# Kernel tuning notes

Measured on AMD Instinct MI355X. Metric: run time of the kernel, lower is better.

## Reference

```python
import jax, jax.numpy as jnp
import numpy as np
import math

SR = 96000.0
FRAME = 2048
NB = 16
GAIN_RANGE = (-24.0, 24.0)
Q_RANGE = (0.5, 16.0)
BROADBAND = (-60.0, 0.0)
HPF_R = (20.0, 500.0)
LPF_R = (5000.0, 20000.0)
SHELF_R = (50.0, 16000.0)
PEAK_R = (100.0, 15000.0)


def _dfreq(n, rng):
    lo, hi = math.log(rng[0]), math.log(rng[1])
    return jnp.exp(lo + n * (hi - lo))


def _dgain(n, rng=GAIN_RANGE):
    return rng[0] + n * (rng[1] - rng[0])


def _dq(n):
    lo, hi = math.log(Q_RANGE[0]), math.log(Q_RANGE[1])
    return jnp.exp(lo + n * (hi - lo))


def _coeffs(ftype, fc, gain_db, Q):
    # returns stacked [g, k, a1, a2, a3, m0, m1, m2], each same shape as fc
    g = jnp.clip(jnp.tan(math.pi * fc / SR), 1e-6, 100.0)
    Q = jnp.clip(Q, 0.1, 100.0)
    one = jnp.ones_like(g)
    zero = jnp.zeros_like(g)
    if ftype in ('highpass', 'lowpass'):
        k = 1.0 / Q
        a1 = 1.0 / (1.0 + g * (g + k)); a2 = g * a1; a3 = g * a2
        if ftype == 'highpass':
            m0, m1, m2 = one, -k, -one
        else:
            m0, m1, m2 = zero, zero, one
    elif ftype == 'peak':
        A = jnp.power(10.0, gain_db / 40.0)
        k = jnp.where(gain_db >= 0, 1.0 / (Q * A), A / Q)
        a1 = 1.0 / (1.0 + g * (g + k)); a2 = g * a1; a3 = g * a2
        m0, m1, m2 = one, k * (A * A - 1.0), zero
    elif ftype == 'lowshelf':
        A = jnp.power(10.0, gain_db / 40.0); sA = jnp.sqrt(A); k = 1.0 / Q
        gs = jnp.where(gain_db >= 0, g / sA, g * sA)
        a1 = 1.0 / (1.0 + gs * (gs + k)); a2 = gs * a1; a3 = gs * a2
        m0, m1, m2 = one, k * (A - 1.0), A * A - 1.0
    else:  # highshelf
        A = jnp.power(10.0, gain_db / 40.0); sA = jnp.sqrt(A); k = 1.0 / Q
        gs = jnp.where(gain_db >= 0, g * sA, g / sA)
        a1 = 1.0 / (1.0 + gs * (gs + k)); a2 = gs * a1; a3 = gs * a2
        m0, m1, m2 = A * A, k * (1.0 - A) * A, 1.0 - A * A
    return jnp.stack([g, k, a1, a2, a3, m0, m1, m2], 0)


def _all_coeffs(params, n_frames_audio):
    # params: (B, 50, n_frames_params) -> coeffs (nF, NB, 8, B), in/out gains (nF, B)
    B = params.shape[0]
    nFp = params.shape[2]
    pidx = jnp.minimum(jnp.arange(n_frames_audio), nFp - 1)
    fp = jnp.take(params, pidx, axis=2)                 # (B, 50, nF)
    bq = fp[:, :NB * 3, :].reshape(B, NB, 3, n_frames_audio)
    in_g = jnp.power(10.0, _dgain(fp[:, -2, :], BROADBAND) / 20.0)   # (B, nF)
    out_g = jnp.power(10.0, _dgain(fp[:, -1, :], BROADBAND) / 20.0)  # (B, nF)
    cs = []
    for i in range(NB):
        fn, gn, qn = bq[:, i, 0], bq[:, i, 1], bq[:, i, 2]  # (B, nF)
        Q = _dq(qn)
        if i == 0:
            c = _coeffs('highpass', _dfreq(fn, HPF_R), None, Q)
        elif i == 15:
            c = _coeffs('lowpass', _dfreq(fn, LPF_R), None, Q)
        elif i == 1:
            c = _coeffs('lowshelf', _dfreq(fn, SHELF_R), _dgain(gn), Q)
        elif i == 14:
            c = _coeffs('highshelf', _dfreq(fn, SHELF_R), _dgain(gn), Q)
        else:
            c = _coeffs('peak', _dfreq(fn, PEAK_R), _dgain(gn), Q)
        cs.append(c)  # (8, B, nF)
    coeffs = jnp.transpose(jnp.stack(cs, 0), (3, 0, 1, 2))  # (nF, NB, 8, B)
    return coeffs, in_g.T, out_g.T


def _forward(audio, params):
    B, S = audio.shape
    nF = S // FRAME  # S chosen as exact multiple of FRAME
    coeffs, in_g, out_g = _all_coeffs(params, nF)
    frames = jnp.transpose(audio.reshape(B, nF, FRAME), (1, 2, 0))  # (nF, FRAME, B)

    def frame_step(states, xs):
        fr, c, ig, og = xs  # fr (FRAME,B), c (NB,8,B), ig (B,), og (B,)
        x = fr * ig[None, :]
        new_states = []
        for i in range(NB):
            a1, a2, a3 = c[i, 2], c[i, 3], c[i, 4]
            m0, m1, m2 = c[i, 5], c[i, 6], c[i, 7]

            def samp(st, xn, a1=a1, a2=a2, a3=a3, m0=m0, m1=m1, m2=m2):
                ic1, ic2 = st
                v3 = xn - ic2
                v1 = a1 * ic1 + a2 * v3
                v2 = ic2 + a2 * v1 + a3 * v3
                out = m0 * xn + m1 * v1 + m2 * v2
                return (2.0 * v1 - ic1, 2.0 * v2 - ic2), out

            (ic1, ic2), x = jax.lax.scan(samp, (states[i, 0], states[i, 1]), x)
            new_states.append(jnp.stack([ic1, ic2], 0))
        return jnp.stack(new_states, 0), x * og[None, :]

    init = jnp.zeros((NB, 2, B), audio.dtype)
    _, out = jax.lax.scan(frame_step, init, (frames, coeffs, in_g, out_g))
    return jnp.transpose(out, (2, 0, 1)).reshape(B, S)  # (B, S)


_forward_jit = jax.jit(_forward)


def setup_inputs() -> dict:
    key = jax.random.key(0)
    k1, k2 = jax.random.split(key)
    B, S, nFp = 32, 49152, 24  # 24 frames of 2048 samples
    audio = jax.random.normal(k1, (B, S), dtype=jnp.float32) * 0.1
    params = jax.random.uniform(k2, (B, 50, nFp), dtype=jnp.float32)
    return {'audio': audio, 'params': params}


def reference(audio, params):
    return _forward_jit(audio, params)
```

## Files before the change

kernel.cpp:

```cpp
#include <hip/hip_runtime.h>
#include <math.h>

#define NBATCH 32
#define S      49152
#define NF     24
#define NB     16
#define NBLK   4
#define CHUNK  16
#define NCH    768
#define NWAVE  12

__device__ __forceinline__ float clampf(float x, float lo, float hi) {
    return fminf(fmaxf(x, lo), hi);
}

#define FOREACH_S(OP) \
    OP(s00) OP(s01) OP(s02) OP(s03) OP(s04) OP(s05) OP(s06) OP(s07) \
    OP(s08) OP(s09) OP(s10) OP(s11) OP(s12) OP(s13) OP(s14) OP(s15)

#define DECL_S(x) float x;

#define STEPA(x) { \
    const float n1_ = fmaf(t00, ic1, fmaf(t01, ic2, b0 * (x))); \
    const float n2_ = fmaf(t10, ic1, fmaf(t11, ic2, b1 * (x))); \
    ic1 = n1_; ic2 = n2_; }

#define STEPC(x) { \
    const float y_  = fmaf(c0, ic1, fmaf(c1, ic2, c2 * (x))); \
    const float n1_ = fmaf(t00, ic1, fmaf(t01, ic2, b0 * (x))); \
    const float n2_ = fmaf(t10, ic1, fmaf(t11, ic2, b1 * (x))); \
    (x) = y_; ic1 = n1_; ic2 = n2_; }

__global__ __launch_bounds__(NCH, 3)
void biquad_chain_kernel(const float* __restrict__ audio,
                         const float* __restrict__ params,
                         float* __restrict__ out,
                         unsigned int* __restrict__ ws)
{
    __shared__ float sc[NB][NF][16];
    __shared__ float sgain[2][NF];
    __shared__ float4 saggM[NWAVE];
    __shared__ float  saggC[NWAVE][2];
    __shared__ float  sv[NWAVE][2];

    const int t       = threadIdx.x;
    const int xcd     = blockIdx.x & 7;
    const int slot_   = blockIdx.x >> 3;
    const int bt      = xcd * 4 + (slot_ & 3);
    const int quarter = slot_ >> 2;
    const int lane    = t & 63;
    const int wave    = t >> 6;
    const int frame   = quarter * 6 + (wave >> 1);

    if (t < NB * NF) {
        const int f  = t / NF;
        const int fr = t % NF;
        const float* P = params + (size_t)bt * 50 * NF;
        const float fn = P[(3 * f + 0) * NF + fr];
        const float gn = P[(3 * f + 1) * NF + fr];
        const float qn = P[(3 * f + 2) * NF + fr];

        float Q = __expf(-0.69314718f + qn * 3.4657359f);
        Q = clampf(Q, 0.1f, 100.0f);

        float lo, hi;
        int type;
        if      (f == 0)  { lo = 20.0f;   hi = 500.0f;   type = 0; }
        else if (f == 15) { lo = 5000.0f; hi = 20000.0f; type = 1; }
        else if (f == 1)  { lo = 50.0f;   hi = 16000.0f; type = 3; }
        else if (f == 14) { lo = 50.0f;   hi = 16000.0f; type = 4; }
        else              { lo = 100.0f;  hi = 15000.0f; type = 2; }

        const float fc = __expf(__logf(lo) + fn * (__logf(hi) - __logf(lo)));
        float g_ = __tanf((float)M_PI * fc / 96000.0f);
        g_ = clampf(g_, 1e-6f, 100.0f);
        const float gdb = -24.0f + 48.0f * gn;

        float a1, a2, a3, m0, m1, m2;
        if (type == 0 || type == 1) {
            const float k = 1.0f / Q;
            a1 = 1.0f / (1.0f + g_ * (g_ + k)); a2 = g_ * a1; a3 = g_ * a2;
            if (type == 0) { m0 = 1.0f; m1 = -k;   m2 = -1.0f; }
            else           { m0 = 0.0f; m1 = 0.0f; m2 = 1.0f;  }
        } else if (type == 2) {
            const float A = __expf(gdb * (2.30258509f / 40.0f));
            const float k = (gdb >= 0.0f) ? 1.0f / (Q * A) : A / Q;
            a1 = 1.0f / (1.0f + g_ * (g_ + k)); a2 = g_ * a1; a3 = g_ * a2;
            m0 = 1.0f; m1 = k * (A * A - 1.0f); m2 = 0.0f;
        } else {
            const float A  = __expf(gdb * (2.30258509f / 40.0f));
            const float sA = sqrtf(A);
            const float k  = 1.0f / Q;
            float gs;
            if (type == 3) gs = (gdb >= 0.0f) ? g_ / sA : g_ * sA;
            else           gs = (gdb >= 0.0f) ? g_ * sA : g_ / sA;
            a1 = 1.0f / (1.0f + gs * (gs + k)); a2 = gs * a1; a3 = gs * a2;
            if (type == 3) { m0 = 1.0f;  m1 = k * (A - 1.0f);      m2 = A * A - 1.0f; }
            else           { m0 = A * A; m1 = k * (1.0f - A) * A;  m2 = 1.0f - A * A; }
        }

        const float q2  = a2 * a2 + a3;
        const float t00 = 2.0f * a1 - 1.0f;
        const float t01 = -2.0f * a2;
        const float t10 = 2.0f * a1 * a2;
        const float t11 = 1.0f - 2.0f * q2;
        const float b0  = 2.0f * a2;
        const float b1  = 2.0f * q2;
        const float c0  = a1 * (m1 + m2 * a2);
        const float c1  = m2 * (1.0f - q2) - m1 * a2;
        const float c2  = m0 + m1 * a2 + m2 * q2;

        float u00 = t00, u01 = t01, u10 = t10, u11 = t11;
        #pragma unroll
        for (int i = 0; i < 4; i++) {
            const float n00 = u00 * u00 + u01 * u10;
            const float n01 = u00 * u01 + u01 * u11;
            const float n10 = u10 * u00 + u11 * u10;
            const float n11 = u10 * u01 + u11 * u11;
            u00 = n00; u01 = n01; u10 = n10; u11 = n11;
        }

        sc[f][fr][0] = t00; sc[f][fr][1] = t01; sc[f][fr][2] = t10; sc[f][fr][3] = t11;
        sc[f][fr][4] = b0;  sc[f][fr][5] = b1;  sc[f][fr][6] = c0;  sc[f][fr][7] = c1;
        sc[f][fr][8] = c2;  sc[f][fr][9] = u00; sc[f][fr][10] = u01; sc[f][fr][11] = u10;
        sc[f][fr][12] = u11;
    }
    if (t >= 384 && t < 384 + 2 * NF) {
        const int idx = t - 384;
        const int which = idx / NF;
        const int fr    = idx % NF;
        const float* P = params + (size_t)bt * 50 * NF;
        const float p  = P[(48 + which) * NF + fr];
        const float db = -60.0f + 60.0f * p;
        sgain[which][fr] = __expf(db * (2.30258509f / 20.0f));
    }
    __syncthreads();

    FOREACH_S(DECL_S)
    {
        const float ing = sgain[0][frame];
        const float* base = audio + (size_t)bt * S
                          + (size_t)(quarter * NCH + t) * CHUNK;
        float4 q;
        q = *(const float4*)(base +  0); s00 = q.x*ing; s01 = q.y*ing; s02 = q.z*ing; s03 = q.w*ing;
        q = *(const float4*)(base +  4); s04 = q.x*ing; s05 = q.y*ing; s06 = q.z*ing; s07 = q.w*ing;
        q = *(const float4*)(base +  8); s08 = q.x*ing; s09 = q.y*ing; s10 = q.z*ing; s11 = q.w*ing;
        q = *(const float4*)(base + 12); s12 = q.x*ing; s13 = q.y*ing; s14 = q.z*ing; s15 = q.w*ing;
    }

    #pragma unroll 1
    for (int f = 0; f < NB; f++) {
        const float4 q0 = *(const float4*)&sc[f][frame][0];
        const float4 q1 = *(const float4*)&sc[f][frame][4];
        const float4 q2 = *(const float4*)&sc[f][frame][8];
        const float  M11v = sc[f][frame][12];
        const float t00 = q0.x, t01 = q0.y, t10 = q0.z, t11 = q0.w;
        const float b0  = q1.x, b1  = q1.y, c0  = q1.z, c1  = q1.w;
        const float c2  = q2.x;

        float ic1 = 0.0f, ic2 = 0.0f;
        FOREACH_S(STEPA)

        float Md00 = q2.y, Md01 = q2.z, Md10 = q2.w, Md11 = M11v;
        float Ac0 = ic1, Ac1 = ic2;
        #pragma unroll
        for (int d = 1; d < 64; d <<= 1) {
            const float lc0 = __shfl_up(Ac0, d);
            const float lc1 = __shfl_up(Ac1, d);
            if (lane >= d) {
                Ac0 = fmaf(Md00, lc0, fmaf(Md01, lc1, Ac0));
                Ac1 = fmaf(Md10, lc0, fmaf(Md11, lc1, Ac1));
            }
            const float n00 = Md00 * Md00 + Md01 * Md10;
            const float n01 = Md00 * Md01 + Md01 * Md11;
            const float n10 = Md10 * Md00 + Md11 * Md10;
            const float n11 = Md10 * Md01 + Md11 * Md11;
            Md00 = n00; Md01 = n01; Md10 = n10; Md11 = n11;
        }

        if (lane == 63) {
            saggM[wave] = make_float4(Md00, Md01, Md10, Md11);
            saggC[wave][0] = Ac0; saggC[wave][1] = Ac1;
        }
        __syncthreads();

        const unsigned int tag = (unsigned int)(f + 1);
        unsigned int* stagebase = ws + ((bt * NB + f) * NBLK) * 8;

        if (wave == 0) {
            float G00 = 1.0f, G01 = 0.0f, G10 = 0.0f, G11 = 1.0f, Gc0 = 0.0f, Gc1 = 0.0f;
            if (lane < NWAVE) {
                const float4 m = saggM[lane];
                G00 = m.x; G01 = m.y; G10 = m.z; G11 = m.w;
                Gc0 = saggC[lane][0]; Gc1 = saggC[lane][1];
            }
            #pragma unroll
            for (int d = 1; d < 16; d <<= 1) {
                const float l00 = __shfl_up(G00, d);
                const float l01 = __shfl_up(G01, d);
                const float l10 = __shfl_up(G10, d);
                const float l11 = __shfl_up(G11, d);
                const float lc0 = __shfl_up(Gc0, d);
                const float lc1 = __shfl_up(Gc1, d);
                if (lane >= d && lane < NWAVE) {
                    const float n00 = G00 * l00 + G01 * l10;
                    const float n01 = G00 * l01 + G01 * l11;
                    const float n10 = G10 * l00 + G11 * l10;
                    const float n11 = G10 * l01 + G11 * l11;
                    const float nc0 = G00 * lc0 + G01 * lc1 + Gc0;
                    const float nc1 = G10 * lc0 + G11 * lc1 + Gc1;
                    G00 = n00; G01 = n01; G10 = n10; G11 = n11;
                    Gc0 = nc0; Gc1 = nc1;
                }
            }

            if (quarter < NBLK - 1 && lane == NWAVE - 1) {
                unsigned int* slot = stagebase + quarter * 8;
                float* dp = (float*)(slot + 1);
                __hip_atomic_store(&dp[0], G00, __ATOMIC_RELAXED, __HIP_MEMORY_SCOPE_AGENT);
                __hip_atomic_store(&dp[1], G01, __ATOMIC_RELAXED, __HIP_MEMORY_SCOPE_AGENT);
                __hip_atomic_store(&dp[2], G10, __ATOMIC_RELAXED, __HIP_MEMORY_SCOPE_AGENT);
                __hip_atomic_store(&dp[3], G11, __ATOMIC_RELAXED, __HIP_MEMORY_SCOPE_AGENT);
                __hip_atomic_store(&dp[4], Gc0, __ATOMIC_RELAXED, __HIP_MEMORY_SCOPE_AGENT);
                __hip_atomic_store(&dp[5], Gc1, __ATOMIC_RELAXED, __HIP_MEMORY_SCOPE_AGENT);
                __hip_atomic_store(slot, tag, __ATOMIC_RELEASE, __HIP_MEMORY_SCOPE_AGENT);
            }

            float P00 = __shfl_up(G00, 1);
            float P01 = __shfl_up(G01, 1);
            float P10 = __shfl_up(G10, 1);
            float P11 = __shfl_up(G11, 1);
            float Pc0 = __shfl_up(Gc0, 1);
            float Pc1 = __shfl_up(Gc1, 1);
            if (lane == 0) { P00 = 1.0f; P01 = 0.0f; P10 = 0.0f; P11 = 1.0f; Pc0 = 0.0f; Pc1 = 0.0f; }

            float S0x = 0.0f, S0y = 0.0f;
            if (lane == 0 && quarter > 0) {
                float sx = 0.0f, sy = 0.0f;
                for (int k2 = 0; k2 < quarter; k2++) {
                    unsigned int* slot = stagebase + k2 * 8;
                    while (__hip_atomic_load(slot, __ATOMIC_ACQUIRE, __HIP_MEMORY_SCOPE_AGENT) != tag) {
                        __builtin_amdgcn_s_sleep(1);
                    }
                    float* dp = (float*)(slot + 1);
                    const float m00 = __hip_atomic_load(&dp[0], __ATOMIC_RELAXED, __HIP_MEMORY_SCOPE_AGENT);
                    const float m01 = __hip_atomic_load(&dp[1], __ATOMIC_RELAXED, __HIP_MEMORY_SCOPE_AGENT);
                    const float m10 = __hip_atomic_load(&dp[2], __ATOMIC_RELAXED, __HIP_MEMORY_SCOPE_AGENT);
                    const float m11 = __hip_atomic_load(&dp[3], __ATOMIC_RELAXED, __HIP_MEMORY_SCOPE_AGENT);
                    const float cc0 = __hip_atomic_load(&dp[4], __ATOMIC_RELAXED, __HIP_MEMORY_SCOPE_AGENT);
                    const float cc1 = __hip_atomic_load(&dp[5], __ATOMIC_RELAXED, __HIP_MEMORY_SCOPE_AGENT);
                    const float nx = m00 * sx + m01 * sy + cc0;
                    const float ny = m10 * sx + m11 * sy + cc1;
                    sx = nx; sy = ny;
                }
                S0x = sx; S0y = sy;
            }
            S0x = __shfl(S0x, 0);
            S0y = __shfl(S0y, 0);

            if (lane < NWAVE) {
                sv[lane][0] = fmaf(P00, S0x, fmaf(P01, S0y, Pc0));
                sv[lane][1] = fmaf(P10, S0x, fmaf(P11, S0y, Pc1));
            }
        }
        __syncthreads();

        const float vx = sv[wave][0];
        const float vy = sv[wave][1];

        float ce0 = __shfl_up(Ac0, 1);
        float ce1 = __shfl_up(Ac1, 1);
        if (lane == 0) { ce0 = 0.0f; ce1 = 0.0f; }

        float w0 = vx, w1 = vy;
        float p00 = q2.y, p01 = q2.z, p10 = q2.w, p11 = M11v;
        #pragma unroll
        for (int b = 0; b < 6; b++) {
            if (lane & (1 << b)) {
                const float nw0 = fmaf(p00, w0, p01 * w1);
                const float nw1 = fmaf(p10, w0, p11 * w1);
                w0 = nw0; w1 = nw1;
            }
            if (b < 5) {
                const float n00 = p00 * p00 + p01 * p10;
                const float n01 = p00 * p01 + p01 * p11;
                const float n10 = p10 * p00 + p11 * p10;
                const float n11 = p10 * p01 + p11 * p11;
                p00 = n00; p01 = n01; p10 = n10; p11 = n11;
            }
        }
        ic1 = w0 + ce0;
        ic2 = w1 + ce1;

        FOREACH_S(STEPC)
    }

    {
        const float og = sgain[1][frame];
        float* base = out + (size_t)bt * S + (size_t)(quarter * NCH + t) * CHUNK;
        float4 q;
        q.x = s00*og; q.y = s01*og; q.z = s02*og; q.w = s03*og; *(float4*)(base +  0) = q;
        q.x = s04*og; q.y = s05*og; q.z = s06*og; q.w = s07*og; *(float4*)(base +  4) = q;
        q.x = s08*og; q.y = s09*og; q.z = s10*og; q.w = s11*og; *(float4*)(base +  8) = q;
        q.x = s12*og; q.y = s13*og; q.z = s14*og; q.w = s15*og; *(float4*)(base + 12) = q;
    }
}

extern "C" void kernel_launch(void* const* d_in, const int* in_sizes, int n_in,
                              void* d_out, int out_size, void* d_ws, size_t ws_size,
                              hipStream_t stream)
{
    const float* audio  = (const float*)d_in[0];
    const float* params = (const float*)d_in[1];
    float* out = (float*)d_out;
    unsigned int* ws = (unsigned int*)d_ws;
    biquad_chain_kernel<<<NBLK * NBATCH, NCH, 0, stream>>>(audio, params, out, ws);
}
```

Before: 124.8 us.

## Fuse biquad sections pairwise into 4-state block-triangular scan

New measurement: 128.5 us. +3.0%, slower.

```diff
diff --git a/kernel.cpp b/kernel.cpp
--- a/kernel.cpp
+++ b/kernel.cpp
@@ -5,6 +5,7 @@
 #define S      49152
 #define NF     24
 #define NB     16
+#define NPAIR  8
 #define NBLK   4
 #define CHUNK  16
 #define NCH    768
@@ -20,16 +21,44 @@
 
 #define DECL_S(x) float x;
 
-#define STEPA(x) { \
-    const float n1_ = fmaf(t00, ic1, fmaf(t01, ic2, b0 * (x))); \
-    const float n2_ = fmaf(t10, ic1, fmaf(t11, ic2, b1 * (x))); \
-    ic1 = n1_; ic2 = n2_; }
-
-#define STEPC(x) { \
-    const float y_  = fmaf(c0, ic1, fmaf(c1, ic2, c2 * (x))); \
-    const float n1_ = fmaf(t00, ic1, fmaf(t01, ic2, b0 * (x))); \
-    const float n2_ = fmaf(t10, ic1, fmaf(t11, ic2, b1 * (x))); \
-    (x) = y_; ic1 = n1_; ic2 = n2_; }
+#define STEPA2(x) { \
+    const float y1_ = fmaf(c0f, zu, fmaf(c1f, zw, c2f * (x))); \
+    const float nu_ = fmaf(tf00, zu, fmaf(tf01, zw, bf0 * (x))); \
+    const float nw_ = fmaf(tf10, zu, fmaf(tf11, zw, bf1 * (x))); \
+    const float ng_ = fmaf(tg00, zg, fmaf(tg01, zh, bg0 * y1_)); \
+    const float nh_ = fmaf(tg10, zg, fmaf(tg11, zh, bg1 * y1_)); \
+    zu = nu_; zw = nw_; zg = ng_; zh = nh_; }
+
+#define STEPC2(x) { \
+    const float y1_ = fmaf(c0f, zu, fmaf(c1f, zw, c2f * (x))); \
+    const float y2_ = fmaf(c0g, zg, fmaf(c1g, zh, c2g * y1_)); \
+    const float nu_ = fmaf(tf00, zu, fmaf(tf01, zw, bf0 * (x))); \
+    const float nw_ = fmaf(tf10, zu, fmaf(tf11, zw, bf1 * (x))); \
+    const float ng_ = fmaf(tg00, zg, fmaf(tg01, zh, bg0 * y1_)); \
+    const float nh_ = fmaf(tg10, zg, fmaf(tg11, zh, bg1 * y1_)); \
+    (x) = y2_; zu = nu_; zw = nw_; zg = ng_; zh = nh_; }
+
+__device__ __forceinline__ void tri_sq(
+    float& a00, float& a01, float& a10, float& a11,
+    float& b00, float& b01, float& b10, float& b11,
+    float& d00, float& d01, float& d10, float& d11)
+{
+    const float na00 = a00*a00 + a01*a10;
+    const float na01 = a00*a01 + a01*a11;
+    const float na10 = a10*a00 + a11*a10;
+    const float na11 = a10*a01 + a11*a11;
+    const float nb00 = b00*a00 + b01*a10 + d00*b00 + d01*b10;
+    const float nb01 = b00*a01 + b01*a11 + d00*b01 + d01*b11;
+    const float nb10 = b10*a00 + b11*a10 + d10*b00 + d11*b10;
+    const float nb11 = b10*a01 + b11*a11 + d10*b01 + d11*b11;
+    const float nd00 = d00*d00 + d01*d10;
+    const float nd01 = d00*d01 + d01*d11;
+    const float nd10 = d10*d00 + d11*d10;
+    const float nd11 = d10*d01 + d11*d11;
+    a00=na00; a01=na01; a10=na10; a11=na11;
+    b00=nb00; b01=nb01; b10=nb10; b11=nb11;
+    d00=nd00; d01=nd01; d10=nd10; d11=nd11;
+}
 
 __global__ __launch_bounds__(NCH, 3)
 void biquad_chain_kernel(const float* __restrict__ audio,
@@ -37,11 +66,11 @@
                          float* __restrict__ out,
                          unsigned int* __restrict__ ws)
 {
-    __shared__ float sc[NB][NF][16];
+    __shared__ float sfilt[NB][NF][12];
+    __shared__ float spair[NPAIR][NF][48];
     __shared__ float sgain[2][NF];
-    __shared__ float4 saggM[NWAVE];
-    __shared__ float  saggC[NWAVE][2];
-    __shared__ float  sv[NWAVE][2];
+    __shared__ float saggC[NWAVE][4];
+    __shared__ float sv[NWAVE][4];
 
     const int t       = threadIdx.x;
     const int xcd     = blockIdx.x & 7;
@@ -100,30 +129,15 @@
         }
 
         const float q2  = a2 * a2 + a3;
-        const float t00 = 2.0f * a1 - 1.0f;
-        const float t01 = -2.0f * a2;
-        const float t10 = 2.0f * a1 * a2;
-        const float t11 = 1.0f - 2.0f * q2;
-        const float b0  = 2.0f * a2;
-        const float b1  = 2.0f * q2;
-        const float c0  = a1 * (m1 + m2 * a2);
-        const float c1  = m2 * (1.0f - q2) - m1 * a2;
-        const float c2  = m0 + m1 * a2 + m2 * q2;
-
-        float u00 = t00, u01 = t01, u10 = t10, u11 = t11;
-        #pragma unroll
-        for (int i = 0; i < 4; i++) {
-            const float n00 = u00 * u00 + u01 * u10;
-            const float n01 = u00 * u01 + u01 * u11;
-            const float n10 = u10 * u00 + u11 * u10;
-            const float n11 = u10 * u01 + u11 * u11;
-            u00 = n00; u01 = n01; u10 = n10; u11 = n11;
-        }
-
-        sc[f][fr][0] = t00; sc[f][fr][1] = t01; sc[f][fr][2] = t10; sc[f][fr][3] = t11;
-        sc[f][fr][4] = b0;  sc[f][fr][5] = b1;  sc[f][fr][6] = c0;  sc[f][fr][7] = c1;
-        sc[f][fr][8] = c2;  sc[f][fr][9] = u00; sc[f][fr][10] = u01; sc[f][fr][11] = u10;
-        sc[f][fr][12] = u11;
+        sfilt[f][fr][0] = 2.0f * a1 - 1.0f;
+        sfilt[f][fr][1] = -2.0f * a2;
+        sfilt[f][fr][2] = 2.0f * a1 * a2;
+        sfilt[f][fr][3] = 1.0f - 2.0f * q2;
+        sfilt[f][fr][4] = 2.0f * a2;
+        sfilt[f][fr][5] = 2.0f * q2;
+        sfilt[f][fr][6] = a1 * (m1 + m2 * a2);
+        sfilt[f][fr][7] = m2 * (1.0f - q2) - m1 * a2;
+        sfilt[f][fr][8] = m0 + m1 * a2 + m2 * q2;
     }
     if (t >= 384 && t < 384 + 2 * NF) {
         const int idx = t - 384;
@@ -133,6 +147,37 @@
         const float p  = P[(48 + which) * NF + fr];
         const float db = -60.0f + 60.0f * p;
         sgain[which][fr] = __expf(db * (2.30258509f / 20.0f));
+    }
+    __syncthreads();
+
+    if (t < NPAIR * NF) {
+        const int p  = t / NF;
+        const int fr = t % NF;
+        const float* F0 = sfilt[2 * p][fr];
+        const float* F1 = sfilt[2 * p + 1][fr];
+        float* W = spair[p][fr];
+        W[0]=F0[0]; W[1]=F0[1]; W[2]=F0[2]; W[3]=F0[3];
+        W[4]=F0[4]; W[5]=F0[5]; W[6]=F0[6]; W[7]=F0[7];
+        W[8]=F0[8]; W[9]=F1[0]; W[10]=F1[1]; W[11]=F1[2];
+        W[12]=F1[3]; W[13]=F1[4]; W[14]=F1[5]; W[15]=F1[6];
+        W[16]=F1[7]; W[17]=F1[8]; W[18]=0.0f; W[19]=0.0f;
+
+        float a00=F0[0], a01=F0[1], a10=F0[2], a11=F0[3];
+        float b00=F1[4]*F0[6], b01=F1[4]*F0[7];
+        float b10=F1[5]*F0[6], b11=F1[5]*F0[7];
+        float d00=F1[0], d01=F1[1], d10=F1[2], d11=F1[3];
+        #pragma unroll
+        for (int i = 0; i < 4; i++)
+            tri_sq(a00,a01,a10,a11,b00,b01,b10,b11,d00,d01,d10,d11);
+        W[20]=a00; W[21]=a01; W[22]=a10; W[23]=a11;
+        W[24]=b00; W[25]=b01; W[26]=b10; W[27]=b11;
+        W[28]=d00; W[29]=d01; W[30]=d10; W[31]=d11;
+        #pragma unroll
+        for (int i = 0; i < 6; i++)
+            tri_sq(a00,a01,a10,a11,b00,b01,b10,b11,d00,d01,d10,d11);
+        W[32]=a00; W[33]=a01; W[34]=a10; W[35]=a11;
+        W[36]=b00; W[37]=b01; W[38]=b10; W[39]=b11;
+        W[40]=d00; W[41]=d01; W[42]=d10; W[43]=d11;
     }
     __syncthreads();
 
@@ -149,150 +194,212 @@
     }
 
     #pragma unroll 1
-    for (int f = 0; f < NB; f++) {
-        const float4 q0 = *(const float4*)&sc[f][frame][0];
-        const float4 q1 = *(const float4*)&sc[f][frame][4];
-        const float4 q2 = *(const float4*)&sc[f][frame][8];
-        const float  M11v = sc[f][frame][12];
-        const float t00 = q0.x, t01 = q0.y, t10 = q0.z, t11 = q0.w;
-        const float b0  = q1.x, b1  = q1.y, c0  = q1.z, c1  = q1.w;
-        const float c2  = q2.x;
-
-        float ic1 = 0.0f, ic2 = 0.0f;
-        FOREACH_S(STEPA)
-
-        float Md00 = q2.y, Md01 = q2.z, Md10 = q2.w, Md11 = M11v;
-        float Ac0 = ic1, Ac1 = ic2;
+    for (int p = 0; p < NPAIR; p++) {
+        const float* W = spair[p][frame];
+        const float4 q0 = *(const float4*)&W[0];
+        const float4 q1 = *(const float4*)&W[4];
+        const float4 q2 = *(const float4*)&W[8];
+        const float4 q3 = *(const float4*)&W[12];
+        const float4 q4 = *(const float4*)&W[16];
+        const float tf00=q0.x, tf01=q0.y, tf10=q0.z, tf11=q0.w;
+        const float bf0=q1.x, bf1=q1.y, c0f=q1.z, c1f=q1.w;
+        const float c2f=q2.x, tg00=q2.y, tg01=q2.z, tg10=q2.w;
+        const float tg11=q3.x, bg0=q3.y, bg1=q3.z, c0g=q3.w;
+        const float c1g=q4.x, c2g=q4.y;
+
+        float zu = 0.0f, zw = 0.0f, zg = 0.0f, zh = 0.0f;
+        FOREACH_S(STEPA2)
+        float cx0 = zu, cx1 = zw, cx2 = zg, cx3 = zh;
+
+        float ma00, ma01, ma10, ma11, mb00, mb01, mb10, mb11, md00, md01, md10, md11;
+        {
+            const float4 m0v = *(const float4*)&W[20];
+            const float4 m1v = *(const float4*)&W[24];
+            const float4 m2v = *(const float4*)&W[28];
+            ma00=m0v.x; ma01=m0v.y; ma10=m0v.z; ma11=m0v.w;
+            mb00=m1v.x; mb01=m1v.y; mb10=m1v.z; mb11=m1v.w;
+            md00=m2v.x; md01=m2v.y; md10=m2v.z; md11=m2v.w;
+        }
         #pragma unroll
         for (int d = 1; d < 64; d <<= 1) {
-            const float lc0 = __shfl_up(Ac0, d);
-            const float lc1 = __shfl_up(Ac1, d);
+            const float l0 = __shfl_up(cx0, d);
+            const float l1 = __shfl_up(cx1, d);
+            const float l2 = __shfl_up(cx2, d);
+            const float l3 = __shfl_up(cx3, d);
             if (lane >= d) {
-                Ac0 = fmaf(Md00, lc0, fmaf(Md01, lc1, Ac0));
-                Ac1 = fmaf(Md10, lc0, fmaf(Md11, lc1, Ac1));
-            }
-            const float n00 = Md00 * Md00 + Md01 * Md10;
-            const float n01 = Md00 * Md01 + Md01 * Md11;
-            const float n10 = Md10 * Md00 + Md11 * Md10;
-            const float n11 = Md10 * Md01 + Md11 * Md11;
-            Md00 = n00; Md01 = n01; Md10 = n10; Md11 = n11;
+                cx0 = fmaf(ma00, l0, fmaf(ma01, l1, cx0));
+                cx1 = fmaf(ma10, l0, fmaf(ma11, l1, cx1));
+                cx2 = fmaf(mb00, l0, fmaf(mb01, l1, fmaf(md00, l2, fmaf(md01, l3, cx2))));
+                cx3 = fmaf(mb10, l0, fmaf(mb11, l1, fmaf(md10, l2, fmaf(md11, l3, cx3))));
+            }
+            if (d < 32)
+                tri_sq(ma00,ma01,ma10,ma11,mb00,mb01,mb10,mb11,md00,md01,md10,md11);
         }
 
         if (lane == 63) {
-            saggM[wave] = make_float4(Md00, Md01, Md10, Md11);
-            saggC[wave][0] = Ac0; saggC[wave][1] = Ac1;
+            *(float4*)saggC[wave] = make_float4(cx0, cx1, cx2, cx3);
         }
         __syncthreads();
 
-        const unsigned int tag = (unsigned int)(f + 1);
-        unsigned int* stagebase = ws + ((bt * NB + f) * NBLK) * 8;
+        const unsigned int tag = (unsigned int)(p + 1);
+        unsigned int* stagebase = ws + (((bt * NPAIR + p) * NBLK)) * 20;
 
         if (wave == 0) {
-            float G00 = 1.0f, G01 = 0.0f, G10 = 0.0f, G11 = 1.0f, Gc0 = 0.0f, Gc1 = 0.0f;
+            float Ga00=1.0f,Ga01=0.0f,Ga10=0.0f,Ga11=1.0f;
+            float Gb00=0.0f,Gb01=0.0f,Gb10=0.0f,Gb11=0.0f;
+            float Gd00=1.0f,Gd01=0.0f,Gd10=0.0f,Gd11=1.0f;
+            float Gc0=0.0f,Gc1=0.0f,Gc2=0.0f,Gc3=0.0f;
             if (lane < NWAVE) {
-                const float4 m = saggM[lane];
-                G00 = m.x; G01 = m.y; G10 = m.z; G11 = m.w;
-                Gc0 = saggC[lane][0]; Gc1 = saggC[lane][1];
+                const float* WM = spair[p][quarter * 6 + (lane >> 1)];
+                const float4 m0v = *(const float4*)&WM[32];
+                const float4 m1v = *(const float4*)&WM[36];
+                const float4 m2v = *(const float4*)&WM[40];
+                Ga00=m0v.x; Ga01=m0v.y; Ga10=m0v.z; Ga11=m0v.w;
+                Gb00=m1v.x; Gb01=m1v.y; Gb10=m1v.z; Gb11=m1v.w;
+                Gd00=m2v.x; Gd01=m2v.y; Gd10=m2v.z; Gd11=m2v.w;
+                const float4 cv = *(const float4*)saggC[lane];
+                Gc0=cv.x; Gc1=cv.y; Gc2=cv.z; Gc3=cv.w;
             }
             #pragma unroll
             for (int d = 1; d < 16; d <<= 1) {
-                const float l00 = __shfl_up(G00, d);
-                const float l01 = __shfl_up(G01, d);
-                const float l10 = __shfl_up(G10, d);
-                const float l11 = __shfl_up(G11, d);
-                const float lc0 = __shfl_up(Gc0, d);
-                const float lc1 = __shfl_up(Gc1, d);
+                const float la00=__shfl_up(Ga00,d), la01=__shfl_up(Ga01,d);
+                const float la10=__shfl_up(Ga10,d), la11=__shfl_up(Ga11,d);
+                const float lb00=__shfl_up(Gb00,d), lb01=__shfl_up(Gb01,d);
+                const float lb10=__shfl_up(Gb10,d), lb11=__shfl_up(Gb11,d);
+                const float ld00=__shfl_up(Gd00,d), ld01=__shfl_up(Gd01,d);
+                const float ld10=__shfl_up(Gd10,d), ld11=__shfl_up(Gd11,d);
+                const float lc0=__shfl_up(Gc0,d), lc1=__shfl_up(Gc1,d);
+                const float lc2=__shfl_up(Gc2,d), lc3=__shfl_up(Gc3,d);
                 if (lane >= d && lane < NWAVE) {
-                    const float n00 = G00 * l00 + G01 * l10;
-                    const float n01 = G00 * l01 + G01 * l11;
-                    const float n10 = G10 * l00 + G11 * l10;
-                    const float n11 = G10 * l01 + G11 * l11;
-                    const float nc0 = G00 * lc0 + G01 * lc1 + Gc0;
-                    const float nc1 = G10 * lc0 + G11 * lc1 + Gc1;
-                    G00 = n00; G01 = n01; G10 = n10; G11 = n11;
-                    Gc0 = nc0; Gc1 = nc1;
+                    const float na00 = Ga00*la00 + Ga01*la10;
+                    const float na01 = Ga00*la01 + Ga01*la11;
+                    const float na10 = Ga10*la00 + Ga11*la10;
+                    const float na11 = Ga10*la01 + Ga11*la11;
+                    const float nb00 = Gb00*la00 + Gb01*la10 + Gd00*lb00 + Gd01*lb10;
+                    const float nb01 = Gb00*la01 + Gb01*la11 + Gd00*lb01 + Gd01*lb11;
+                    const float nb10 = Gb10*la00 + Gb11*la10 + Gd10*lb00 + Gd11*lb10;
+                    const float nb11 = Gb10*la01 + Gb11*la11 + Gd10*lb01 + Gd11*lb11;
+                    const float nd00 = Gd00*ld00 + Gd01*ld10;
+                    const float nd01 = Gd00*ld01 + Gd01*ld11;
+                    const float nd10 = Gd10*ld00 + Gd11*ld10;
+                    const float nd11 = Gd10*ld01 + Gd11*ld11;
+                    const float nc0 = Ga00*lc0 + Ga01*lc1 + Gc0;
+                    const float nc1 = Ga10*lc0 + Ga11*lc1 + Gc1;
+                    const float nc2 = Gb00*lc0 + Gb01*lc1 + Gd00*lc2 + Gd01*lc3 + Gc2;
+                    const float nc3 = Gb10*lc0 + Gb11*lc1 + Gd10*lc2 + Gd11*lc3 + Gc3;
+                    Ga00=na00; Ga01=na01; Ga10=na10; Ga11=na11;
+                    Gb00=nb00; Gb01=nb01; Gb10=nb10; Gb11=nb11;
+                    Gd00=nd00; Gd01=nd01; Gd10=nd10; Gd11=nd11;
+                    Gc0=nc0; Gc1=nc1; Gc2=nc2; Gc3=nc3;
                 }
             }
 
             if (quarter < NBLK - 1 && lane == NWAVE - 1) {
-                unsigned int* slot = stagebase + quarter * 8;
+                unsigned int* slot = stagebase + quarter * 20;
                 float* dp = (float*)(slot + 1);
-                __hip_atomic_store(&dp[0], G00, __ATOMIC_RELAXED, __HIP_MEMORY_SCOPE_AGENT);
-                __hip_atomic_store(&dp[1], G01, __ATOMIC_RELAXED, __HIP_MEMORY_SCOPE_AGENT);
-                __hip_atomic_store(&dp[2], G10, __ATOMIC_RELAXED, __HIP_MEMORY_SCOPE_AGENT);
-                __hip_atomic_store(&dp[3], G11, __ATOMIC_RELAXED, __HIP_MEMORY_SCOPE_AGENT);
-                __hip_atomic_store(&dp[4], Gc0, __ATOMIC_RELAXED, __HIP_MEMORY_SCOPE_AGENT);
-                __hip_atomic_store(&dp[5], Gc1, __ATOMIC_RELAXED, __HIP_MEMORY_SCOPE_AGENT);
+                __hip_atomic_store(&dp[0],  Ga00, __ATOMIC_RELAXED, __HIP_MEMORY_SCOPE_AGENT);
+                __hip_atomic_store(&dp[1],  Ga01, __ATOMIC_RELAXED, __HIP_MEMORY_SCOPE_AGENT);
+                __hip_atomic_store(&dp[2],  Ga10, __ATOMIC_RELAXED, __HIP_MEMORY_SCOPE_AGENT);
+                __hip_atomic_store(&dp[3],  Ga11, __ATOMIC_RELAXED, __HIP_MEMORY_SCOPE_AGENT);
+                __hip_atomic_store(&dp[4],  Gb00, __ATOMIC_RELAXED, __HIP_MEMORY_SCOPE_AGENT);
+                __hip_atomic_store(&dp[5],  Gb01, __ATOMIC_RELAXED, __HIP_MEMORY_SCOPE_AGENT);
+                __hip_atomic_store(&dp[6],  Gb10, __ATOMIC_RELAXED, __HIP_MEMORY_SCOPE_AGENT);
+                __hip_atomic_store(&dp[7],  Gb11, __ATOMIC_RELAXED, __HIP_MEMORY_SCOPE_AGENT);
+                __hip_atomic_store(&dp[8],  Gd00, __ATOMIC_RELAXED, __HIP_MEMORY_SCOPE_AGENT);
+                __hip_atomic_store(&dp[9],  Gd01, __ATOMIC_RELAXED, __HIP_MEMORY_SCOPE_AGENT);
+                __hip_atomic_store(&dp[10], Gd10, __ATOMIC_RELAXED, __HIP_MEMORY_SCOPE_AGENT);
+                __hip_atomic_store(&dp[11], Gd11, __ATOMIC_RELAXED, __HIP_MEMORY_SCOPE_AGENT);
+                __hip_atomic_store(&dp[12], Gc0,  __ATOMIC_RELAXED, __HIP_MEMORY_SCOPE_AGENT);
+                __hip_atomic_store(&dp[13], Gc1,  __ATOMIC_RELAXED, __HIP_MEMORY_SCOPE_AGENT);
+                __hip_atomic_store(&dp[14], Gc2,  __ATOMIC_RELAXED, __HIP_MEMORY_SCOPE_AGENT);
+                __hip_atomic_store(&dp[15], Gc3,  __ATOMIC_RELAXED, __HIP_MEMORY_SCOPE_AGENT);
                 __hip_atomic_store(slot, tag, __ATOMIC_RELEASE, __HIP_MEMORY_SCOPE_AGENT);
             }
 
-            float P00 = __shfl_up(G00, 1);
-            float P01 = __shfl_up(G01, 1);
-            float P10 = __shfl_up(G10, 1);
-            float P11 = __shfl_up(G11, 1);
-            float Pc0 = __shfl_up(Gc0, 1);
-            float Pc1 = __shfl_up(Gc1, 1);
-            if (lane == 0) { P00 = 1.0f; P01 = 0.0f; P10 = 0.0f; P11 = 1.0f; Pc0 = 0.0f; Pc1 = 0.0f; }
-
-            float S0x = 0.0f, S0y = 0.0f;
+            float Pa00=__shfl_up(Ga00,1), Pa01=__shfl_up(Ga01,1);
+            float Pa10=__shfl_up(Ga10,1), Pa11=__shfl_up(Ga11,1);
+            float Pb00=__shfl_up(Gb00,1), Pb01=__shfl_up(Gb01,1);
+            float Pb10=__shfl_up(Gb10,1), Pb11=__shfl_up(Gb11,1);
+            float Pd00=__shfl_up(Gd00,1), Pd01=__shfl_up(Gd01,1);
+            float Pd10=__shfl_up(Gd10,1), Pd11=__shfl_up(Gd11,1);
+            float Pc0=__shfl_up(Gc0,1), Pc1=__shfl_up(Gc1,1);
+            float Pc2=__shfl_up(Gc2,1), Pc3=__shfl_up(Gc3,1);
+            if (lane == 0) {
+                Pa00=1.0f; Pa01=0.0f; Pa10=0.0f; Pa11=1.0f;
+                Pb00=0.0f; Pb01=0.0f; Pb10=0.0f; Pb11=0.0f;
+                Pd00=1.0f; Pd01=0.0f; Pd10=0.0f; Pd11=1.0f;
+                Pc0=0.0f; Pc1=0.0f; Pc2=0.0f; Pc3=0.0f;
+            }
+
+            float S0a=0.0f, S0b=0.0f, S0c=0.0f, S0d=0.0f;
             if (lane == 0 && quarter > 0) {
-                float sx = 0.0f, sy = 0.0f;
+                float sx0=0.0f, sx1=0.0f, sx2=0.0f, sx3=0.0f;
                 for (int k2 = 0; k2 < quarter; k2++) {
-                    unsigned int* slot = stagebase + k2 * 8;
+                    unsigned int* slot = stagebase + k2 * 20;
                     while (__hip_atomic_load(slot, __ATOMIC_ACQUIRE, __HIP_MEMORY_SCOPE_AGENT) != tag) {
                         __builtin_amdgcn_s_sleep(1);
                     }
                     float* dp = (float*)(slot + 1);
-                    const float m00 = __hip_atomic_load(&dp[0], __ATOMIC_RELAXED, __HIP_MEMORY_SCOPE_AGENT);
-                    const float m01 = __hip_atomic_load(&dp[1], __ATOMIC_RELAXED, __HIP_MEMORY_SCOPE_AGENT);
-                    const float m10 = __hip_atomic_load(&dp[2], __ATOMIC_RELAXED, __HIP_MEMORY_SCOPE_AGENT);
-                    const float m11 = __hip_atomic_load(&dp[3], __ATOMIC_RELAXED, __HIP_MEMORY_SCOPE_AGENT);
-                    const float cc0 = __hip_atomic_load(&dp[4], __ATOMIC_RELAXED, __HIP_MEMORY_SCOPE_AGENT);
-                    const float cc1 = __hip_atomic_load(&dp[5], __ATOMIC_RELAXED, __HIP_MEMORY_SCOPE_AGENT);
-                    const float nx = m00 * sx + m01 * sy + cc0;
-                    const float ny = m10 * sx + m11 * sy + cc1;
-                    sx = nx; sy = ny;
+                    float m[16];
+                    #pragma unroll
+                    for (int i = 0; i < 16; i++)
+                        m[i] = __hip_atomic_load(&dp[i], __ATOMIC_RELAXED, __HIP_MEMORY_SCOPE_AGENT);
+                    const float n0 = m[0]*sx0 + m[1]*sx1 + m[12];
+                    const float n1 = m[2]*sx0 + m[3]*sx1 + m[13];
+                    const float n2 = m[4]*sx0 + m[5]*sx1 + m[8]*sx2 + m[9]*sx3 + m[14];
+                    const float n3 = m[6]*sx0 + m[7]*sx1 + m[10]*sx2 + m[11]*sx3 + m[15];
+                    sx0=n0; sx1=n1; sx2=n2; sx3=n3;
                 }
-                S0x = sx; S0y = sy;
-            }
-            S0x = __shfl(S0x, 0);
-            S0y = __shfl(S0y, 0);
+                S0a=sx0; S0b=sx1; S0c=sx2; S0d=sx3;
+            }
+            S0a = __shfl(S0a, 0); S0b = __shfl(S0b, 0);
+            S0c = __shfl(S0c, 0); S0d = __shfl(S0d, 0);
 
             if (lane < NWAVE) {
-                sv[lane][0] = fmaf(P00, S0x, fmaf(P01, S0y, Pc0));
-                sv[lane][1] = fmaf(P10, S0x, fmaf(P11, S0y, Pc1));
+                const float v0 = Pa00*S0a + Pa01*S0b + Pc0;
+                const float v1 = Pa10*S0a + Pa11*S0b + Pc1;
+                const float v2 = Pb00*S0a + Pb01*S0b + Pd00*S0c + Pd01*S0d + Pc2;
+                const float v3 = Pb10*S0a + Pb11*S0b + Pd10*S0c + Pd11*S0d + Pc3;
+                *(float4*)sv[lane] = make_float4(v0, v1, v2, v3);
             }
         }
         __syncthreads();
 
-        const float vx = sv[wave][0];
-        const float vy = sv[wave][1];
-
-        float ce0 = __shfl_up(Ac0, 1);
-        float ce1 = __shfl_up(Ac1, 1);
-        if (lane == 0) { ce0 = 0.0f; ce1 = 0.0f; }
-
-        float w0 = vx, w1 = vy;
-        float p00 = q2.y, p01 = q2.z, p10 = q2.w, p11 = M11v;
-        #pragma unroll
-        for (int b = 0; b < 6; b++) {
-            if (lane & (1 << b)) {
-                const float nw0 = fmaf(p00, w0, p01 * w1);
-                const float nw1 = fmaf(p10, w0, p11 * w1);
-                w0 = nw0; w1 = nw1;
-            }
-            if (b < 5) {
-                const float n00 = p00 * p00 + p01 * p10;
-                const float n01 = p00 * p01 + p01 * p11;
-                const float n10 = p10 * p00 + p11 * p10;
-                const float n11 = p10 * p01 + p11 * p11;
-                p00 = n00; p01 = n01; p10 = n10; p11 = n11;
-            }
-        }
-        ic1 = w0 + ce0;
-        ic2 = w1 + ce1;
-
-        FOREACH_S(STEPC)
+        const float4 vv = *(const float4*)sv[wave];
+
+        float ce0 = __shfl_up(cx0, 1);
+        float ce1 = __shfl_up(cx1, 1);
+        float ce2 = __shfl_up(cx2, 1);
+        float ce3 = __shfl_up(cx3, 1);
+        if (lane == 0) { ce0 = 0.0f; ce1 = 0.0f; ce2 = 0.0f; ce3 = 0.0f; }
+
+        float w0 = vv.x, w1 = vv.y, w2 = vv.z, w3 = vv.w;
+        {
+            const float4 m0v = *(const float4*)&W[20];
+            const float4 m1v = *(const float4*)&W[24];
+            const float4 m2v = *(const float4*)&W[28];
+            float pa00=m0v.x, pa01=m0v.y, pa10=m0v.z, pa11=m0v.w;
+            float pb00=m1v.x, pb01=m1v.y, pb10=m1v.z, pb11=m1v.w;
+            float pd00=m2v.x, pd01=m2v.y, pd10=m2v.z, pd11=m2v.w;
+            #pragma unroll
+            for (int b = 0; b < 6; b++) {
+                if (lane & (1 << b)) {
+                    const float n0 = pa00*w0 + pa01*w1;
+                    const float n1 = pa10*w0 + pa11*w1;
+                    const float n2 = pb00*w0 + pb01*w1 + pd00*w2 + pd01*w3;
+                    const float n3 = pb10*w0 + pb11*w1 + pd10*w2 + pd11*w3;
+                    w0=n0; w1=n1; w2=n2; w3=n3;
+                }
+                if (b < 5)
+                    tri_sq(pa00,pa01,pa10,pa11,pb00,pb01,pb10,pb11,pd00,pd01,pd10,pd11);
+            }
+        }
+        zu = w0 + ce0;
+        zw = w1 + ce1;
+        zg = w2 + ce2;
+        zh = w3 + ce3;
+
+        FOREACH_S(STEPC2)
     }
 
     {
```

## Split each batch across eight blocks and precompute scan matrix powers in LDS

Applied to the files above, without the earlier changes.

Measured after the change: 148.2 us. 1.19x slower.

```diff
diff --git a/kernel.cpp b/kernel.cpp
--- a/kernel.cpp
+++ b/kernel.cpp
@@ -5,8 +5,8 @@
 #define S      49152
 #define NF     24
 #define NB     16
-#define NBLK   4
-#define CHUNK  16
+#define NBLK   8
+#define CHUNK  8
 #define NCH    768
 #define NWAVE  12
 
@@ -15,8 +15,7 @@
 }
 
 #define FOREACH_S(OP) \
-    OP(s00) OP(s01) OP(s02) OP(s03) OP(s04) OP(s05) OP(s06) OP(s07) \
-    OP(s08) OP(s09) OP(s10) OP(s11) OP(s12) OP(s13) OP(s14) OP(s15)
+    OP(s00) OP(s01) OP(s02) OP(s03) OP(s04) OP(s05) OP(s06) OP(s07)
 
 #define DECL_S(x) float x;
 
@@ -37,20 +36,19 @@
                          float* __restrict__ out,
                          unsigned int* __restrict__ ws)
 {
-    __shared__ float sc[NB][NF][16];
+    __shared__ float sc[NB][NF][40];
     __shared__ float sgain[2][NF];
-    __shared__ float4 saggM[NWAVE];
-    __shared__ float  saggC[NWAVE][2];
-    __shared__ float  sv[NWAVE][2];
-
-    const int t       = threadIdx.x;
-    const int xcd     = blockIdx.x & 7;
-    const int slot_   = blockIdx.x >> 3;
-    const int bt      = xcd * 4 + (slot_ & 3);
-    const int quarter = slot_ >> 2;
-    const int lane    = t & 63;
-    const int wave    = t >> 6;
-    const int frame   = quarter * 6 + (wave >> 1);
+    __shared__ float saggC[NWAVE][2];
+    __shared__ float sv[NWAVE][2];
+
+    const int t      = threadIdx.x;
+    const int xcd    = blockIdx.x & 7;
+    const int slot_  = blockIdx.x >> 3;
+    const int bt     = xcd * 4 + (slot_ & 3);
+    const int eighth = slot_ >> 2;
+    const int lane   = t & 63;
+    const int wave   = t >> 6;
+    const int frame  = eighth * 3 + (wave >> 2);
 
     if (t < NB * NF) {
         const int f  = t / NF;
@@ -104,26 +102,34 @@
         const float t01 = -2.0f * a2;
         const float t10 = 2.0f * a1 * a2;
         const float t11 = 1.0f - 2.0f * q2;
-        const float b0  = 2.0f * a2;
-        const float b1  = 2.0f * q2;
-        const float c0  = a1 * (m1 + m2 * a2);
-        const float c1  = m2 * (1.0f - q2) - m1 * a2;
-        const float c2  = m0 + m1 * a2 + m2 * q2;
+
+        sc[f][fr][0] = t00; sc[f][fr][1] = t01; sc[f][fr][2] = t10; sc[f][fr][3] = t11;
+        sc[f][fr][4] = 2.0f * a2;
+        sc[f][fr][5] = 2.0f * q2;
+        sc[f][fr][6] = a1 * (m1 + m2 * a2);
+        sc[f][fr][7] = m2 * (1.0f - q2) - m1 * a2;
+        sc[f][fr][8] = m0 + m1 * a2 + m2 * q2;
 
         float u00 = t00, u01 = t01, u10 = t10, u11 = t11;
         #pragma unroll
-        for (int i = 0; i < 4; i++) {
-            const float n00 = u00 * u00 + u01 * u10;
-            const float n01 = u00 * u01 + u01 * u11;
-            const float n10 = u10 * u00 + u11 * u10;
-            const float n11 = u10 * u01 + u11 * u11;
-            u00 = n00; u01 = n01; u10 = n10; u11 = n11;
-        }
-
-        sc[f][fr][0] = t00; sc[f][fr][1] = t01; sc[f][fr][2] = t10; sc[f][fr][3] = t11;
-        sc[f][fr][4] = b0;  sc[f][fr][5] = b1;  sc[f][fr][6] = c0;  sc[f][fr][7] = c1;
-        sc[f][fr][8] = c2;  sc[f][fr][9] = u00; sc[f][fr][10] = u01; sc[f][fr][11] = u10;
-        sc[f][fr][12] = u11;
+        for (int i = 0; i < 3; i++) {
+            const float n00 = u00*u00 + u01*u10;
+            const float n01 = u00*u01 + u01*u11;
+            const float n10 = u10*u00 + u11*u10;
+            const float n11 = u10*u01 + u11*u11;
+            u00=n00; u01=n01; u10=n10; u11=n11;
+        }
+        sc[f][fr][12] = u00; sc[f][fr][13] = u01; sc[f][fr][14] = u10; sc[f][fr][15] = u11;
+        #pragma unroll
+        for (int j = 1; j <= 6; j++) {
+            const float n00 = u00*u00 + u01*u10;
+            const float n01 = u00*u01 + u01*u11;
+            const float n10 = u10*u00 + u11*u10;
+            const float n11 = u10*u01 + u11*u11;
+            u00=n00; u01=n01; u10=n10; u11=n11;
+            sc[f][fr][12+4*j] = u00; sc[f][fr][13+4*j] = u01;
+            sc[f][fr][14+4*j] = u10; sc[f][fr][15+4*j] = u11;
+        }
     }
     if (t >= 384 && t < 384 + 2 * NF) {
         const int idx = t - 384;
@@ -140,46 +146,37 @@
     {
         const float ing = sgain[0][frame];
         const float* base = audio + (size_t)bt * S
-                          + (size_t)(quarter * NCH + t) * CHUNK;
+                          + (size_t)(eighth * NCH + t) * CHUNK;
         float4 q;
-        q = *(const float4*)(base +  0); s00 = q.x*ing; s01 = q.y*ing; s02 = q.z*ing; s03 = q.w*ing;
-        q = *(const float4*)(base +  4); s04 = q.x*ing; s05 = q.y*ing; s06 = q.z*ing; s07 = q.w*ing;
-        q = *(const float4*)(base +  8); s08 = q.x*ing; s09 = q.y*ing; s10 = q.z*ing; s11 = q.w*ing;
-        q = *(const float4*)(base + 12); s12 = q.x*ing; s13 = q.y*ing; s14 = q.z*ing; s15 = q.w*ing;
+        q = *(const float4*)(base + 0); s00 = q.x*ing; s01 = q.y*ing; s02 = q.z*ing; s03 = q.w*ing;
+        q = *(const float4*)(base + 4); s04 = q.x*ing; s05 = q.y*ing; s06 = q.z*ing; s07 = q.w*ing;
     }
 
     #pragma unroll 1
     for (int f = 0; f < NB; f++) {
         const float4 q0 = *(const float4*)&sc[f][frame][0];
         const float4 q1 = *(const float4*)&sc[f][frame][4];
-        const float4 q2 = *(const float4*)&sc[f][frame][8];
-        const float  M11v = sc[f][frame][12];
         const float t00 = q0.x, t01 = q0.y, t10 = q0.z, t11 = q0.w;
         const float b0  = q1.x, b1  = q1.y, c0  = q1.z, c1  = q1.w;
-        const float c2  = q2.x;
+        const float c2  = sc[f][frame][8];
 
         float ic1 = 0.0f, ic2 = 0.0f;
         FOREACH_S(STEPA)
 
-        float Md00 = q2.y, Md01 = q2.z, Md10 = q2.w, Md11 = M11v;
         float Ac0 = ic1, Ac1 = ic2;
         #pragma unroll
-        for (int d = 1; d < 64; d <<= 1) {
+        for (int i = 0; i < 6; i++) {
+            const int d = 1 << i;
+            const float4 mv = *(const float4*)&sc[f][frame][12 + 4*i];
             const float lc0 = __shfl_up(Ac0, d);
             const float lc1 = __shfl_up(Ac1, d);
             if (lane >= d) {
-                Ac0 = fmaf(Md00, lc0, fmaf(Md01, lc1, Ac0));
-                Ac1 = fmaf(Md10, lc0, fmaf(Md11, lc1, Ac1));
-            }
-            const float n00 = Md00 * Md00 + Md01 * Md10;
-            const float n01 = Md00 * Md01 + Md01 * Md11;
-            const float n10 = Md10 * Md00 + Md11 * Md10;
-            const float n11 = Md10 * Md01 + Md11 * Md11;
-            Md00 = n00; Md01 = n01; Md10 = n10; Md11 = n11;
+                Ac0 = fmaf(mv.x, lc0, fmaf(mv.y, lc1, Ac0));
+                Ac1 = fmaf(mv.z, lc0, fmaf(mv.w, lc1, Ac1));
+            }
         }
 
         if (lane == 63) {
-            saggM[wave] = make_float4(Md00, Md01, Md10, Md11);
             saggC[wave][0] = Ac0; saggC[wave][1] = Ac1;
         }
         __syncthreads();
@@ -190,7 +187,7 @@
         if (wave == 0) {
             float G00 = 1.0f, G01 = 0.0f, G10 = 0.0f, G11 = 1.0f, Gc0 = 0.0f, Gc1 = 0.0f;
             if (lane < NWAVE) {
-                const float4 m = saggM[lane];
+                const float4 m = *(const float4*)&sc[f][eighth * 3 + (lane >> 2)][36];
                 G00 = m.x; G01 = m.y; G10 = m.z; G11 = m.w;
                 Gc0 = saggC[lane][0]; Gc1 = saggC[lane][1];
             }
@@ -214,8 +211,8 @@
                 }
             }
 
-            if (quarter < NBLK - 1 && lane == NWAVE - 1) {
-                unsigned int* slot = stagebase + quarter * 8;
+            if (eighth < NBLK - 1 && lane == NWAVE - 1) {
+                unsigned int* slot = stagebase + eighth * 8;
                 float* dp = (float*)(slot + 1);
                 __hip_atomic_store(&dp[0], G00, __ATOMIC_RELAXED, __HIP_MEMORY_SCOPE_AGENT);
                 __hip_atomic_store(&dp[1], G01, __ATOMIC_RELAXED, __HIP_MEMORY_SCOPE_AGENT);
@@ -226,6 +223,46 @@
                 __hip_atomic_store(slot, tag, __ATOMIC_RELEASE, __HIP_MEMORY_SCOPE_AGENT);
             }
 
+            float Fm00 = 1.0f, Fm01 = 0.0f, Fm10 = 0.0f, Fm11 = 1.0f;
+            float Fc0 = 0.0f, Fc1 = 0.0f;
+            if (lane < eighth) {
+                unsigned int* slot = stagebase + lane * 8;
+                while (__hip_atomic_load(slot, __ATOMIC_ACQUIRE, __HIP_MEMORY_SCOPE_AGENT) != tag) {
+                    __builtin_amdgcn_s_sleep(1);
+                }
+                float* dp = (float*)(slot + 1);
+                Fm00 = __hip_atomic_load(&dp[0], __ATOMIC_RELAXED, __HIP_MEMORY_SCOPE_AGENT);
+                Fm01 = __hip_atomic_load(&dp[1], __ATOMIC_RELAXED, __HIP_MEMORY_SCOPE_AGENT);
+                Fm10 = __hip_atomic_load(&dp[2], __ATOMIC_RELAXED, __HIP_MEMORY_SCOPE_AGENT);
+                Fm11 = __hip_atomic_load(&dp[3], __ATOMIC_RELAXED, __HIP_MEMORY_SCOPE_AGENT);
+                Fc0  = __hip_atomic_load(&dp[4], __ATOMIC_RELAXED, __HIP_MEMORY_SCOPE_AGENT);
+                Fc1  = __hip_atomic_load(&dp[5], __ATOMIC_RELAXED, __HIP_MEMORY_SCOPE_AGENT);
+            }
+            #pragma unroll
+            for (int d = 1; d < 8; d <<= 1) {
+                const float l00 = __shfl_up(Fm00, d);
+                const float l01 = __shfl_up(Fm01, d);
+                const float l10 = __shfl_up(Fm10, d);
+                const float l11 = __shfl_up(Fm11, d);
+                const float lc0 = __shfl_up(Fc0, d);
+                const float lc1 = __shfl_up(Fc1, d);
+                if (lane >= d && lane < 8) {
+                    const float n00 = Fm00 * l00 + Fm01 * l10;
+                    const float n01 = Fm00 * l01 + Fm01 * l11;
+                    const float n10 = Fm10 * l00 + Fm11 * l10;
+                    const float n11 = Fm10 * l01 + Fm11 * l11;
+                    const float nc0 = Fm00 * lc0 + Fm01 * lc1 + Fc0;
+                    const float nc1 = Fm10 * lc0 + Fm11 * lc1 + Fc1;
+                    Fm00 = n00; Fm01 = n01; Fm10 = n10; Fm11 = n11;
+                    Fc0 = nc0; Fc1 = nc1;
+                }
+            }
+            float S0x = 0.0f, S0y = 0.0f;
+            if (eighth > 0) {
+                S0x = __shfl(Fc0, eighth - 1);
+                S0y = __shfl(Fc1, eighth - 1);
+            }
+
             float P00 = __shfl_up(G00, 1);
             float P01 = __shfl_up(G01, 1);
             float P10 = __shfl_up(G10, 1);
@@ -234,30 +271,6 @@
             float Pc1 = __shfl_up(Gc1, 1);
             if (lane == 0) { P00 = 1.0f; P01 = 0.0f; P10 = 0.0f; P11 = 1.0f; Pc0 = 0.0f; Pc1 = 0.0f; }
 
-            float S0x = 0.0f, S0y = 0.0f;
-            if (lane == 0 && quarter > 0) {
-                float sx = 0.0f, sy = 0.0f;
-                for (int k2 = 0; k2 < quarter; k2++) {
-                    unsigned int* slot = stagebase + k2 * 8;
-                    while (__hip_atomic_load(slot, __ATOMIC_ACQUIRE, __HIP_MEMORY_SCOPE_AGENT) != tag) {
-                        __builtin_amdgcn_s_sleep(1);
-                    }
-                    float* dp = (float*)(slot + 1);
-                    const float m00 = __hip_atomic_load(&dp[0], __ATOMIC_RELAXED, __HIP_MEMORY_SCOPE_AGENT);
-                    const float m01 = __hip_atomic_load(&dp[1], __ATOMIC_RELAXED, __HIP_MEMORY_SCOPE_AGENT);
-                    const float m10 = __hip_atomic_load(&dp[2], __ATOMIC_RELAXED, __HIP_MEMORY_SCOPE_AGENT);
-                    const float m11 = __hip_atomic_load(&dp[3], __ATOMIC_RELAXED, __HIP_MEMORY_SCOPE_AGENT);
-                    const float cc0 = __hip_atomic_load(&dp[4], __ATOMIC_RELAXED, __HIP_MEMORY_SCOPE_AGENT);
-                    const float cc1 = __hip_atomic_load(&dp[5], __ATOMIC_RELAXED, __HIP_MEMORY_SCOPE_AGENT);
-                    const float nx = m00 * sx + m01 * sy + cc0;
-                    const float ny = m10 * sx + m11 * sy + cc1;
-                    sx = nx; sy = ny;
-                }
-                S0x = sx; S0y = sy;
-            }
-            S0x = __shfl(S0x, 0);
-            S0y = __shfl(S0y, 0);
-
             if (lane < NWAVE) {
                 sv[lane][0] = fmaf(P00, S0x, fmaf(P01, S0y, Pc0));
                 sv[lane][1] = fmaf(P10, S0x, fmaf(P11, S0y, Pc1));
@@ -273,20 +286,13 @@
         if (lane == 0) { ce0 = 0.0f; ce1 = 0.0f; }
 
         float w0 = vx, w1 = vy;
-        float p00 = q2.y, p01 = q2.z, p10 = q2.w, p11 = M11v;
         #pragma unroll
         for (int b = 0; b < 6; b++) {
             if (lane & (1 << b)) {
-                const float nw0 = fmaf(p00, w0, p01 * w1);
-                const float nw1 = fmaf(p10, w0, p11 * w1);
-                w0 = nw0; w1 = nw1;
-            }
-            if (b < 5) {
-                const float n00 = p00 * p00 + p01 * p10;
-                const float n01 = p00 * p01 + p01 * p11;
-                const float n10 = p10 * p00 + p11 * p10;
-                const float n11 = p10 * p01 + p11 * p11;
-                p00 = n00; p01 = n01; p10 = n10; p11 = n11;
+                const float4 mv = *(const float4*)&sc[f][frame][12 + 4*b];
+                const float n0 = fmaf(mv.x, w0, mv.y * w1);
+                const float n1 = fmaf(mv.z, w0, mv.w * w1);
+                w0 = n0; w1 = n1;
             }
         }
         ic1 = w0 + ce0;
@@ -297,12 +303,10 @@
 
     {
         const float og = sgain[1][frame];
-        float* base = out + (size_t)bt * S + (size_t)(quarter * NCH + t) * CHUNK;
+        float* base = out + (size_t)bt * S + (size_t)(eighth * NCH + t) * CHUNK;
         float4 q;
-        q.x = s00*og; q.y = s01*og; q.z = s02*og; q.w = s03*og; *(float4*)(base +  0) = q;
-        q.x = s04*og; q.y = s05*og; q.z = s06*og; q.w = s07*og; *(float4*)(base +  4) = q;
-        q.x = s08*og; q.y = s09*og; q.z = s10*og; q.w = s11*og; *(float4*)(base +  8) = q;
-        q.x = s12*og; q.y = s13*og; q.z = s14*og; q.w = s15*og; *(float4*)(base + 12) = q;
+        q.x = s00*og; q.y = s01*og; q.z = s02*og; q.w = s03*og; *(float4*)(base + 0) = q;
+        q.x = s04*og; q.y = s05*og; q.z = s06*og; q.w = s07*og; *(float4*)(base + 4) = q;
     }
 }
 
```
